# Optimization experiments

Hardware: AMD Instinct MI355X
Metric: run time of the kernel (lower is better)

## Reference

```python
import jax, jax.numpy as jnp
import numpy as np

B, N, D = 4, 1024, 1024      # batch, seq_len, d_model
H, DK, DV = 16, 64, 64       # n_head, d_k, d_v


def setup_inputs() -> dict:
    key = jax.random.key(0)
    ks = jax.random.split(key, 6)
    xavier = (2.0 / (D + DK)) ** 0.5  # xavier_normal_ std for (d_model, d_k) fan
    return {
        "q": jax.random.normal(ks[0], (B, N, D), jnp.float32),
        "k": jax.random.normal(ks[1], (B, N, D), jnp.float32),
        "v": jax.random.normal(ks[2], (B, N, D), jnp.float32),
        "weight_qs": xavier * jax.random.normal(ks[3], (H, D, DK), jnp.float32),
        "weight_ks": xavier * jax.random.normal(ks[4], (H, D, DK), jnp.float32),
        "weight_vs": xavier * jax.random.normal(ks[5], (H, D, DV), jnp.float32),
    }


def reference(q, k, v, weight_qs, weight_ks, weight_vs):
    # Per-head projections (torch: repeat batch over heads + bmm with (H,D,DK) weights)
    h, d_model, d_k = weight_qs.shape
    scale = 1.0 / (d_k ** 0.5)
    qh = jnp.einsum('bnd,hdk->hbnk', q, weight_qs)   # (H,B,N,DK)
    kh = jnp.einsum('bmd,hdk->hbmk', k, weight_ks)   # (H,B,M,DK)
    vh = jnp.einsum('bmd,hdv->hbmv', v, weight_vs)   # (H,B,M,DV)
    scores = jnp.einsum('hbnk,hbmk->hbnm', qh, kh) * scale  # (H,B,N,M)
    attn = jax.nn.softmax(scores, axis=-1)
    # dropout is identity in eval/deterministic mode
    out = jnp.einsum('hbnm,hbmv->hbnv', attn, vh)    # (H,B,N,DV)
    # torch: split head-stacked batch dim and cat along feature dim -> (B,N,H*DV)
    out = jnp.transpose(out, (1, 2, 0, 3)).reshape(out.shape[1], out.shape[2], -1)
    attn = attn.reshape(h * attn.shape[1], attn.shape[2], attn.shape[3])  # (H*B,N,M)
    return out, attn
```

## Files before the change

### kernel.cpp

```cpp
#include <hip/hip_runtime.h>

typedef short short8 __attribute__((ext_vector_type(8)));
typedef short short4_ __attribute__((ext_vector_type(4)));
typedef float f32x4 __attribute__((ext_vector_type(4)));

#define GLD16(gsrc, ldst) \
  __builtin_amdgcn_global_load_lds((__attribute__((address_space(1))) const void*)(gsrc), \
                                   (__attribute__((address_space(3))) void*)(ldst), 16, 0, 0)

#define BAR() do { asm volatile("s_waitcnt lgkmcnt(0)" ::: "memory"); \
  __builtin_amdgcn_sched_barrier(0); __builtin_amdgcn_s_barrier(); } while (0)

static __device__ __forceinline__ short f2bf(float f) {
  union { float f; unsigned u; } x; x.f = f;
  unsigned r = x.u + 0x7fffu + ((x.u >> 16) & 1u);
  return (short)(r >> 16);
}
static __device__ __forceinline__ float bf2f(unsigned short h) {
  union { unsigned u; float f; } x; x.u = ((unsigned)h) << 16;
  return x.f;
}

__global__ __launch_bounds__(256) void cast_qkv(
    const float* __restrict__ q, const float* __restrict__ k, const float* __restrict__ v,
    short* __restrict__ xq, short* __restrict__ xk, short* __restrict__ xv) {
  int z = blockIdx.z;
  const float* s = (z == 0) ? q : (z == 1) ? k : v;
  short* d = (z == 0) ? xq : (z == 1) ? xk : xv;
  int i = (blockIdx.x * 256 + threadIdx.x) * 4;
  float4 f = *(const float4*)(s + i);
  short4_ o;
  o[0] = f2bf(f.x); o[1] = f2bf(f.y); o[2] = f2bf(f.z); o[3] = f2bf(f.w);
  *(short4_*)(d + i) = o;
}

__global__ __launch_bounds__(256) void pack_w(
    const float* __restrict__ wq, const float* __restrict__ wk, const float* __restrict__ wv,
    short* __restrict__ oq, short* __restrict__ ok, short* __restrict__ ov) {
  int z = blockIdx.z;
  const float* W = (z == 0) ? wq : (z == 1) ? wk : wv;
  short* o = ((z == 0) ? oq : (z == 1) ? ok : ov) + (size_t)blockIdx.x * 1024;
  int c = blockIdx.x;
  int h = c >> 6, kk = c & 63;
  const float* src = W + (size_t)h * 65536 + kk;
  #pragma unroll
  for (int it = 0; it < 4; ++it) {
    int d = it * 256 + threadIdx.x;
    o[d] = f2bf(src[(size_t)d * 64]);
  }
}

__global__ __launch_bounds__(256) void proj_gemm(
    const short* __restrict__ xq, const short* __restrict__ xk, const short* __restrict__ xv,
    const short* __restrict__ wq, const short* __restrict__ wk, const short* __restrict__ wv,
    short* __restrict__ pq, short* __restrict__ pk, short* __restrict__ pv) {
  int z = blockIdx.z;
  const short* A  = (z == 0) ? xq : (z == 1) ? xk : xv;
  const short* Bt = (z == 0) ? wq : (z == 1) ? wk : wv;
  short* C        = (z == 0) ? pq : (z == 1) ? pk : pv;
  __shared__ __attribute__((aligned(16))) short As[128 * 32];
  __shared__ __attribute__((aligned(16))) short Bs[128 * 32];
  int t = threadIdx.x, l = t & 63, w = t >> 6;
  int wr = w >> 1, wc = w & 1;
  int lr = l & 15, lk = l >> 4;
  int bm0 = blockIdx.y * 128, bn0 = blockIdx.x * 128;
  const f32x4 Z = {0.f, 0.f, 0.f, 0.f};
  f32x4 acc[4][4];
  #pragma unroll
  for (int m = 0; m < 4; ++m)
    #pragma unroll
    for (int n = 0; n < 4; ++n) acc[m][n] = Z;

  int boff0 = w * 2 * 1024 + l * 16;
  int row0 = boff0 >> 6, ke0 = (boff0 & 63) >> 1;
  int boff1 = boff0 + 1024;
  int row1 = boff1 >> 6, ke1 = (boff1 & 63) >> 1;
  const short* ga0 = A + (size_t)(bm0 + row0) * 1024 + ke0;
  const short* ga1 = A + (size_t)(bm0 + row1) * 1024 + ke1;
  const short* gb0 = Bt + (size_t)(bn0 + row0) * 1024 + ke0;
  const short* gb1 = Bt + (size_t)(bn0 + row1) * 1024 + ke1;
  short* lA0 = As + (w * 2) * 512;     short* lA1 = As + (w * 2 + 1) * 512;
  short* lB0 = Bs + (w * 2) * 512;     short* lB1 = Bs + (w * 2 + 1) * 512;

  for (int kb = 0; kb < 1024; kb += 32) {
    GLD16(ga0 + kb, lA0);
    GLD16(ga1 + kb, lA1);
    GLD16(gb0 + kb, lB0);
    GLD16(gb1 + kb, lB1);
    __syncthreads();
    short8 a[4], bfr[4];
    #pragma unroll
    for (int m = 0; m < 4; ++m)
      a[m] = *(const short8*)(As + (wr * 64 + m * 16 + lr) * 32 + lk * 8);
    #pragma unroll
    for (int n = 0; n < 4; ++n)
      bfr[n] = *(const short8*)(Bs + (wc * 64 + n * 16 + lr) * 32 + lk * 8);
    __builtin_amdgcn_s_setprio(1);
    #pragma unroll
    for (int m = 0; m < 4; ++m)
      #pragma unroll
      for (int n = 0; n < 4; ++n)
        acc[m][n] = __builtin_amdgcn_mfma_f32_16x16x32_bf16(a[m], bfr[n], acc[m][n], 0, 0, 0);
    __builtin_amdgcn_s_setprio(0);
    __syncthreads();
  }
  #pragma unroll
  for (int m = 0; m < 4; ++m)
    #pragma unroll
    for (int n = 0; n < 4; ++n)
      #pragma unroll
      for (int i = 0; i < 4; ++i) {
        int r = bm0 + wr * 64 + m * 16 + lk * 4 + i;
        int cc = bn0 + wc * 64 + n * 16 + lr;
        C[(size_t)r * 1024 + cc] = f2bf(acc[m][n][i]);
      }
}

__global__ __launch_bounds__(256) void vtrans(
    const short* __restrict__ pv, short* __restrict__ vt) {
  __shared__ short T[64 * 72];
  int t = threadIdx.x;
  int hb = blockIdx.y, h = hb >> 2, b = hb & 3;
  int n0 = blockIdx.x * 64;
  const short* src = pv + (size_t)b * 1048576 + (size_t)n0 * 1024 + h * 64;
  #pragma unroll
  for (int it = 0; it < 2; ++it) {
    int id = it * 256 + t;
    int row = id >> 3, seg = id & 7;
    *(short8*)(T + row * 72 + seg * 8) = *(const short8*)(src + (size_t)row * 1024 + seg * 8);
  }
  __syncthreads();
  short* dst = vt + (size_t)hb * 65536 + n0;
  #pragma unroll
  for (int it = 0; it < 2; ++it) {
    int id = it * 256 + t;
    int dv = id >> 3, seg = id & 7;
    short8 vv;
    #pragma unroll
    for (int jj = 0; jj < 8; ++jj) vv[jj] = T[(seg * 8 + jj) * 72 + dv];
    *(short8*)(dst + (size_t)dv * 1024 + seg * 8) = vv;
  }
}

#define PW 72
__global__ __launch_bounds__(512) void attn_fused(
    const short* __restrict__ pq, const short* __restrict__ pk, const short* __restrict__ vt,
    float* __restrict__ dout) {
  __shared__ __attribute__((aligned(16))) short Ks[2][64 * PW];
  __shared__ __attribute__((aligned(16))) short Vs[2][64 * PW];
  __shared__ __attribute__((aligned(16))) short Ps[128 * PW];
  int t = threadIdx.x, l = t & 63, w = t >> 6;
  int lr = l & 15, lk = l >> 4;
  int bid = blockIdx.x;
  int swz = (bid & 7) * 64 + (bid >> 3);
  int hb = swz >> 3, qt = swz & 7;
  int h = hb >> 2, b = hb & 3;
  int q0 = qt * 128;
  const short* Qg = pq + (size_t)b * 1048576 + h * 64;
  const short* Kg = pk + (size_t)b * 1048576 + h * 64;
  const short* Vt = vt + (size_t)hb * 65536;
  float* attnp = dout + 4194304 + (size_t)hb * 1048576;
  const f32x4 Z = {0.f, 0.f, 0.f, 0.f};
  const float scale = 0.125f;
  int r0 = w * 16;
  int sj = t >> 3, sco = (t & 7) * 8;

  const short* qrow = Qg + (size_t)(q0 + r0 + lr) * 1024;
  short8 aq[2];
  aq[0] = *(const short8*)(qrow + lk * 8);
  aq[1] = *(const short8*)(qrow + 32 + lk * 8);

  short8 ka, va;
  ka = *(const short8*)(Kg + (size_t)sj * 1024 + sco);
  *(short8*)(Ks[0] + sj * PW + sco) = ka;
  BAR();

  float s[4] = {0.f, 0.f, 0.f, 0.f};

  for (int nc = 0; nc < 16; ++nc) {
    int cur = nc & 1;
    if (nc < 15)
      ka = *(const short8*)(Kg + (size_t)((nc + 1) * 64 + sj) * 1024 + sco);
    f32x4 acc[4] = {Z, Z, Z, Z};
    __builtin_amdgcn_s_setprio(1);
    #pragma unroll
    for (int kk = 0; kk < 2; ++kk)
      #pragma unroll
      for (int n = 0; n < 4; ++n) {
        short8 bk = *(const short8*)(Ks[cur] + (n * 16 + lr) * PW + kk * 32 + lk * 8);
        acc[n] = __builtin_amdgcn_mfma_f32_16x16x32_bf16(aq[kk], bk, acc[n], 0, 0, 0);
      }
    __builtin_amdgcn_s_setprio(0);
    #pragma unroll
    for (int i = 0; i < 4; ++i)
      s[i] += __expf(acc[0][i] * scale) + __expf(acc[1][i] * scale) +
              __expf(acc[2][i] * scale) + __expf(acc[3][i] * scale);
    if (nc < 15)
      *(short8*)(Ks[cur ^ 1] + sj * PW + sco) = ka;
    BAR();
  }
  #pragma unroll
  for (int i = 0; i < 4; ++i)
    #pragma unroll
    for (int msk = 1; msk < 16; msk <<= 1)
      s[i] += __shfl_xor(s[i], msk, 64);
  float inv[4];
  #pragma unroll
  for (int i = 0; i < 4; ++i) inv[i] = 1.0f / s[i];

  ka = *(const short8*)(Kg + (size_t)sj * 1024 + sco);
  va = *(const short8*)(Vt + (size_t)sj * 1024 + sco);
  *(short8*)(Ks[0] + sj * PW + sco) = ka;
  *(short8*)(Vs[0] + sj * PW + sco) = va;
  BAR();

  f32x4 acco[4] = {Z, Z, Z, Z};
  int prow = r0 + (l >> 2), pseg = (l & 3) * 16;
  float* gpb = attnp + (size_t)(q0 + prow) * 1024 + pseg;
  for (int nc = 0; nc < 16; ++nc) {
    int cur = nc & 1;
    if (nc < 15) {
      ka = *(const short8*)(Kg + (size_t)((nc + 1) * 64 + sj) * 1024 + sco);
      va = *(const short8*)(Vt + (size_t)sj * 1024 + (nc + 1) * 64 + sco);
    }
    f32x4 acc[4] = {Z, Z, Z, Z};
    __builtin_amdgcn_s_setprio(1);
    #pragma unroll
    for (int kk = 0; kk < 2; ++kk)
      #pragma unroll
      for (int n = 0; n < 4; ++n) {
        short8 bk = *(const short8*)(Ks[cur] + (n * 16 + lr) * PW + kk * 32 + lk * 8);
        acc[n] = __builtin_amdgcn_mfma_f32_16x16x32_bf16(aq[kk], bk, acc[n], 0, 0, 0);
      }
    __builtin_amdgcn_s_setprio(0);
    #pragma unroll
    for (int n = 0; n < 4; ++n)
      #pragma unroll
      for (int i = 0; i < 4; ++i) {
        float p = __expf(acc[n][i] * scale) * inv[i];
        Ps[(r0 + lk * 4 + i) * PW + n * 16 + lr] = f2bf(p);
      }
    #pragma unroll
    for (int kk = 0; kk < 2; ++kk) {
      short8 ap = *(const short8*)(Ps + (r0 + lr) * PW + kk * 32 + lk * 8);
      __builtin_amdgcn_s_setprio(1);
      #pragma unroll
      for (int f = 0; f < 4; ++f) {
        short8 bv = *(const short8*)(Vs[cur] + (f * 16 + lr) * PW + kk * 32 + lk * 8);
        acco[f] = __builtin_amdgcn_mfma_f32_16x16x32_bf16(ap, bv, acco[f], 0, 0, 0);
      }
      __builtin_amdgcn_s_setprio(0);
    }
    {
      short8 p0 = *(const short8*)(Ps + prow * PW + pseg);
      short8 p1 = *(const short8*)(Ps + prow * PW + pseg + 8);
      float* gp = gpb + nc * 64;
      float4 f0 = {bf2f((unsigned short)p0[0]), bf2f((unsigned short)p0[1]),
                   bf2f((unsigned short)p0[2]), bf2f((unsigned short)p0[3])};
      float4 f1 = {bf2f((unsigned short)p0[4]), bf2f((unsigned short)p0[5]),
                   bf2f((unsigned short)p0[6]), bf2f((unsigned short)p0[7])};
      float4 f2 = {bf2f((unsigned short)p1[0]), bf2f((unsigned short)p1[1]),
                   bf2f((unsigned short)p1[2]), bf2f((unsigned short)p1[3])};
      float4 f3 = {bf2f((unsigned short)p1[4]), bf2f((unsigned short)p1[5]),
                   bf2f((unsigned short)p1[6]), bf2f((unsigned short)p1[7])};
      *(float4*)gp = f0; *(float4*)(gp + 4) = f1;
      *(float4*)(gp + 8) = f2; *(float4*)(gp + 12) = f3;
    }
    if (nc < 15) {
      *(short8*)(Ks[cur ^ 1] + sj * PW + sco) = ka;
      *(short8*)(Vs[cur ^ 1] + sj * PW + sco) = va;
    }
    BAR();
  }
  #pragma unroll
  for (int f = 0; f < 4; ++f)
    #pragma unroll
    for (int i = 0; i < 4; ++i) {
      int row = q0 + r0 + lk * 4 + i;
      int dv = f * 16 + lr;
      dout[(size_t)b * 1048576 + (size_t)row * 1024 + h * 64 + dv] = acco[f][i];
    }
}

extern "C" void kernel_launch(void* const* d_in, const int* in_sizes, int n_in,
                              void* d_out, int out_size, void* d_ws, size_t ws_size,
                              hipStream_t stream) {
  const void* big[3] = {0, 0, 0};
  const void* small[3] = {0, 0, 0};
  int nb = 0, ns = 0;
  for (int i = 0; i < n_in && i < 6; ++i) {
    if (in_sizes[i] == 4194304) { if (nb < 3) big[nb++] = d_in[i]; }
    else                        { if (ns < 3) small[ns++] = d_in[i]; }
  }
  const float *q, *k, *v, *wq, *wk, *wv;
  if (nb == 3 && ns == 3) {
    q = (const float*)big[0]; k = (const float*)big[1]; v = (const float*)big[2];
    wq = (const float*)small[0]; wk = (const float*)small[1]; wv = (const float*)small[2];
  } else {
    q = (const float*)d_in[0]; k = (const float*)d_in[1]; v = (const float*)d_in[2];
    wq = (const float*)d_in[3]; wk = (const float*)d_in[4]; wv = (const float*)d_in[5];
  }
  short* W   = (short*)d_ws;
  short* xq  = W;
  short* xk  = W + 4194304;
  short* xv  = W + 8388608;
  short* wtq = W + 12582912;
  short* wtk = W + 13631488;
  short* wtv = W + 14680064;
  short* pq  = W + 15728640;
  short* pk  = W + 19922944;
  short* pv  = W + 24117248;
  short* vt  = W + 28311552;
  float* out = (float*)d_out;

  cast_qkv<<<dim3(4096, 1, 3), 256, 0, stream>>>(q, k, v, xq, xk, xv);
  pack_w<<<dim3(1024, 1, 3), 256, 0, stream>>>(wq, wk, wv, wtq, wtk, wtv);
  proj_gemm<<<dim3(8, 32, 3), 256, 0, stream>>>(xq, xk, xv, wtq, wtk, wtv, pq, pk, pv);
  vtrans<<<dim3(16, 64), 256, 0, stream>>>(pv, vt);
  attn_fused<<<dim3(512), 512, 0, stream>>>(pq, pk, vt, out);
}
```

Before: 190.8 us.

## Fuse V transpose into projection GEMM epilogue and deepen K/V prefetch

The separate vtrans kernel is removed. The projection GEMM now writes V directly in transposed per-head layout from its epilogue, which saves one kernel launch and a full round trip of the projected V through memory. In the attention kernel, K and V tile loads are now prefetched two tiles ahead through an extra register stage, to hide more global load latency. The transposed epilogue stores are scattered short writes, which may coalesce poorly, and the extra prefetch registers add register pressure.

```diff
diff --git a/kernel.cpp b/kernel.cpp
--- a/kernel.cpp
+++ b/kernel.cpp
@@ -53,11 +53,10 @@
 __global__ __launch_bounds__(256) void proj_gemm(
     const short* __restrict__ xq, const short* __restrict__ xk, const short* __restrict__ xv,
     const short* __restrict__ wq, const short* __restrict__ wk, const short* __restrict__ wv,
-    short* __restrict__ pq, short* __restrict__ pk, short* __restrict__ pv) {
+    short* __restrict__ pq, short* __restrict__ pk, short* __restrict__ vt) {
   int z = blockIdx.z;
   const short* A  = (z == 0) ? xq : (z == 1) ? xk : xv;
   const short* Bt = (z == 0) ? wq : (z == 1) ? wk : wv;
-  short* C        = (z == 0) ? pq : (z == 1) ? pk : pv;
   __shared__ __attribute__((aligned(16))) short As[128 * 32];
   __shared__ __attribute__((aligned(16))) short Bs[128 * 32];
   int t = threadIdx.x, l = t & 63, w = t >> 6;
@@ -112,34 +111,15 @@
       for (int i = 0; i < 4; ++i) {
         int r = bm0 + wr * 64 + m * 16 + lk * 4 + i;
         int cc = bn0 + wc * 64 + n * 16 + lr;
-        C[(size_t)r * 1024 + cc] = f2bf(acc[m][n][i]);
-      }
-}
-
-__global__ __launch_bounds__(256) void vtrans(
-    const short* __restrict__ pv, short* __restrict__ vt) {
-  __shared__ short T[64 * 72];
-  int t = threadIdx.x;
-  int hb = blockIdx.y, h = hb >> 2, b = hb & 3;
-  int n0 = blockIdx.x * 64;
-  const short* src = pv + (size_t)b * 1048576 + (size_t)n0 * 1024 + h * 64;
-  #pragma unroll
-  for (int it = 0; it < 2; ++it) {
-    int id = it * 256 + t;
-    int row = id >> 3, seg = id & 7;
-    *(short8*)(T + row * 72 + seg * 8) = *(const short8*)(src + (size_t)row * 1024 + seg * 8);
-  }
-  __syncthreads();
-  short* dst = vt + (size_t)hb * 65536 + n0;
-  #pragma unroll
-  for (int it = 0; it < 2; ++it) {
-    int id = it * 256 + t;
-    int dv = id >> 3, seg = id & 7;
-    short8 vv;
-    #pragma unroll
-    for (int jj = 0; jj < 8; ++jj) vv[jj] = T[(seg * 8 + jj) * 72 + dv];
-    *(short8*)(dst + (size_t)dv * 1024 + seg * 8) = vv;
-  }
+        short val = f2bf(acc[m][n][i]);
+        if (z == 2) {
+          int b = r >> 10, n1024 = r & 1023, h = cc >> 6, dv = cc & 63;
+          vt[(size_t)(h * 4 + b) * 65536 + (size_t)dv * 1024 + n1024] = val;
+        } else {
+          short* C = (z == 0) ? pq : pk;
+          C[(size_t)r * 1024 + cc] = val;
+        }
+      }
 }
 
 #define PW 72
@@ -170,17 +150,18 @@
   aq[0] = *(const short8*)(qrow + lk * 8);
   aq[1] = *(const short8*)(qrow + 32 + lk * 8);
 
-  short8 ka, va;
-  ka = *(const short8*)(Kg + (size_t)sj * 1024 + sco);
-  *(short8*)(Ks[0] + sj * PW + sco) = ka;
+  short8 ka_w, ka_n, va_w, va_n;
+  ka_w = *(const short8*)(Kg + (size_t)sj * 1024 + sco);
+  *(short8*)(Ks[0] + sj * PW + sco) = ka_w;
+  ka_w = *(const short8*)(Kg + (size_t)(64 + sj) * 1024 + sco);
   BAR();
 
   float s[4] = {0.f, 0.f, 0.f, 0.f};
 
   for (int nc = 0; nc < 16; ++nc) {
     int cur = nc & 1;
-    if (nc < 15)
-      ka = *(const short8*)(Kg + (size_t)((nc + 1) * 64 + sj) * 1024 + sco);
+    if (nc < 14)
+      ka_n = *(const short8*)(Kg + (size_t)((nc + 2) * 64 + sj) * 1024 + sco);
     f32x4 acc[4] = {Z, Z, Z, Z};
     __builtin_amdgcn_s_setprio(1);
     #pragma unroll
@@ -195,8 +176,10 @@
     for (int i = 0; i < 4; ++i)
       s[i] += __expf(acc[0][i] * scale) + __expf(acc[1][i] * scale) +
               __expf(acc[2][i] * scale) + __expf(acc[3][i] * scale);
-    if (nc < 15)
-      *(short8*)(Ks[cur ^ 1] + sj * PW + sco) = ka;
+    if (nc < 15) {
+      *(short8*)(Ks[cur ^ 1] + sj * PW + sco) = ka_w;
+      ka_w = ka_n;
+    }
     BAR();
   }
   #pragma unroll
@@ -208,10 +191,12 @@
   #pragma unroll
   for (int i = 0; i < 4; ++i) inv[i] = 1.0f / s[i];
 
-  ka = *(const short8*)(Kg + (size_t)sj * 1024 + sco);
-  va = *(const short8*)(Vt + (size_t)sj * 1024 + sco);
-  *(short8*)(Ks[0] + sj * PW + sco) = ka;
-  *(short8*)(Vs[0] + sj * PW + sco) = va;
+  ka_w = *(const short8*)(Kg + (size_t)sj * 1024 + sco);
+  va_w = *(const short8*)(Vt + (size_t)sj * 1024 + sco);
+  *(short8*)(Ks[0] + sj * PW + sco) = ka_w;
+  *(short8*)(Vs[0] + sj * PW + sco) = va_w;
+  ka_w = *(const short8*)(Kg + (size_t)(64 + sj) * 1024 + sco);
+  va_w = *(const short8*)(Vt + (size_t)sj * 1024 + 64 + sco);
   BAR();
 
   f32x4 acco[4] = {Z, Z, Z, Z};
@@ -219,9 +204,9 @@
   float* gpb = attnp + (size_t)(q0 + prow) * 1024 + pseg;
   for (int nc = 0; nc < 16; ++nc) {
     int cur = nc & 1;
-    if (nc < 15) {
-      ka = *(const short8*)(Kg + (size_t)((nc + 1) * 64 + sj) * 1024 + sco);
-      va = *(const short8*)(Vt + (size_t)sj * 1024 + (nc + 1) * 64 + sco);
+    if (nc < 14) {
+      ka_n = *(const short8*)(Kg + (size_t)((nc + 2) * 64 + sj) * 1024 + sco);
+      va_n = *(const short8*)(Vt + (size_t)sj * 1024 + (nc + 2) * 64 + sco);
     }
     f32x4 acc[4] = {Z, Z, Z, Z};
     __builtin_amdgcn_s_setprio(1);
@@ -267,8 +252,9 @@
       *(float4*)(gp + 8) = f2; *(float4*)(gp + 12) = f3;
     }
     if (nc < 15) {
-      *(short8*)(Ks[cur ^ 1] + sj * PW + sco) = ka;
-      *(short8*)(Vs[cur ^ 1] + sj * PW + sco) = va;
+      *(short8*)(Ks[cur ^ 1] + sj * PW + sco) = ka_w;
+      *(short8*)(Vs[cur ^ 1] + sj * PW + sco) = va_w;
+      ka_w = ka_n; va_w = va_n;
     }
     BAR();
   }
@@ -309,13 +295,11 @@
   short* wtv = W + 14680064;
   short* pq  = W + 15728640;
   short* pk  = W + 19922944;
-  short* pv  = W + 24117248;
   short* vt  = W + 28311552;
   float* out = (float*)d_out;
 
   cast_qkv<<<dim3(4096, 1, 3), 256, 0, stream>>>(q, k, v, xq, xk, xv);
   pack_w<<<dim3(1024, 1, 3), 256, 0, stream>>>(wq, wk, wv, wtq, wtk, wtv);
-  proj_gemm<<<dim3(8, 32, 3), 256, 0, stream>>>(xq, xk, xv, wtq, wtk, wtv, pq, pk, pv);
-  vtrans<<<dim3(16, 64), 256, 0, stream>>>(pv, vt);
+  proj_gemm<<<dim3(8, 32, 3), 256, 0, stream>>>(xq, xk, xv, wtq, wtk, wtv, pq, pk, vt);
   attn_fused<<<dim3(512), 512, 0, stream>>>(pq, pk, vt, out);
 }
```

Measured after the change: 208.6 us. 1.09x slower.

## Halve attention block to 256 threads with two 16-row tiles per wave

Applied to the files above, without the earlier changes.

Each wave now computes 32 query rows as two 16-row MFMA tiles that share every K and V fragment read from LDS, and the block shrinks from 8 to 4 waves for the same 128-row tile. Each thread stages two short8 chunks of K/V per step instead of one, and the attention-probability writeout covers 32 columns per lane. The aim is to halve the LDS reads of K/V per MFMA and raise instruction-level parallelism per wave. In exchange, register pressure per wave rises and fewer waves are resident to hide latency.

```diff
diff --git a/kernel.cpp b/kernel.cpp
--- a/kernel.cpp
+++ b/kernel.cpp
@@ -143,7 +143,7 @@
 }
 
 #define PW 72
-__global__ __launch_bounds__(512) void attn_fused(
+__global__ __launch_bounds__(256) void attn_fused(
     const short* __restrict__ pq, const short* __restrict__ pk, const short* __restrict__ vt,
     float* __restrict__ dout) {
   __shared__ __attribute__((aligned(16))) short Ks[2][64 * PW];
@@ -162,113 +162,139 @@
   float* attnp = dout + 4194304 + (size_t)hb * 1048576;
   const f32x4 Z = {0.f, 0.f, 0.f, 0.f};
   const float scale = 0.125f;
-  int r0 = w * 16;
-  int sj = t >> 3, sco = (t & 7) * 8;
-
-  const short* qrow = Qg + (size_t)(q0 + r0 + lr) * 1024;
-  short8 aq[2];
-  aq[0] = *(const short8*)(qrow + lk * 8);
-  aq[1] = *(const short8*)(qrow + 32 + lk * 8);
-
-  short8 ka, va;
-  ka = *(const short8*)(Kg + (size_t)sj * 1024 + sco);
-  *(short8*)(Ks[0] + sj * PW + sco) = ka;
+  int r0 = w * 32;
+  int sj = t >> 2, sc0 = (t & 3) * 16;
+
+  const short* qrowA = Qg + (size_t)(q0 + r0 + lr) * 1024;
+  const short* qrowB = Qg + (size_t)(q0 + r0 + 16 + lr) * 1024;
+  short8 aqA[2], aqB[2];
+  aqA[0] = *(const short8*)(qrowA + lk * 8);
+  aqA[1] = *(const short8*)(qrowA + 32 + lk * 8);
+  aqB[0] = *(const short8*)(qrowB + lk * 8);
+  aqB[1] = *(const short8*)(qrowB + 32 + lk * 8);
+
+  short8 ka0, ka1, va0, va1;
+  ka0 = *(const short8*)(Kg + (size_t)sj * 1024 + sc0);
+  ka1 = *(const short8*)(Kg + (size_t)sj * 1024 + sc0 + 8);
+  *(short8*)(Ks[0] + sj * PW + sc0) = ka0;
+  *(short8*)(Ks[0] + sj * PW + sc0 + 8) = ka1;
   BAR();
 
-  float s[4] = {0.f, 0.f, 0.f, 0.f};
+  float sA[4] = {0.f, 0.f, 0.f, 0.f}, sB[4] = {0.f, 0.f, 0.f, 0.f};
 
   for (int nc = 0; nc < 16; ++nc) {
     int cur = nc & 1;
-    if (nc < 15)
-      ka = *(const short8*)(Kg + (size_t)((nc + 1) * 64 + sj) * 1024 + sco);
-    f32x4 acc[4] = {Z, Z, Z, Z};
+    if (nc < 15) {
+      ka0 = *(const short8*)(Kg + (size_t)((nc + 1) * 64 + sj) * 1024 + sc0);
+      ka1 = *(const short8*)(Kg + (size_t)((nc + 1) * 64 + sj) * 1024 + sc0 + 8);
+    }
+    f32x4 accA[4] = {Z, Z, Z, Z}, accB[4] = {Z, Z, Z, Z};
     __builtin_amdgcn_s_setprio(1);
     #pragma unroll
     for (int kk = 0; kk < 2; ++kk)
       #pragma unroll
       for (int n = 0; n < 4; ++n) {
         short8 bk = *(const short8*)(Ks[cur] + (n * 16 + lr) * PW + kk * 32 + lk * 8);
-        acc[n] = __builtin_amdgcn_mfma_f32_16x16x32_bf16(aq[kk], bk, acc[n], 0, 0, 0);
+        accA[n] = __builtin_amdgcn_mfma_f32_16x16x32_bf16(aqA[kk], bk, accA[n], 0, 0, 0);
+        accB[n] = __builtin_amdgcn_mfma_f32_16x16x32_bf16(aqB[kk], bk, accB[n], 0, 0, 0);
       }
     __builtin_amdgcn_s_setprio(0);
     #pragma unroll
-    for (int i = 0; i < 4; ++i)
-      s[i] += __expf(acc[0][i] * scale) + __expf(acc[1][i] * scale) +
-              __expf(acc[2][i] * scale) + __expf(acc[3][i] * scale);
-    if (nc < 15)
-      *(short8*)(Ks[cur ^ 1] + sj * PW + sco) = ka;
+    for (int i = 0; i < 4; ++i) {
+      sA[i] += __expf(accA[0][i] * scale) + __expf(accA[1][i] * scale) +
+               __expf(accA[2][i] * scale) + __expf(accA[3][i] * scale);
+      sB[i] += __expf(accB[0][i] * scale) + __expf(accB[1][i] * scale) +
+               __expf(accB[2][i] * scale) + __expf(accB[3][i] * scale);
+    }
+    if (nc < 15) {
+      *(short8*)(Ks[cur ^ 1] + sj * PW + sc0) = ka0;
+      *(short8*)(Ks[cur ^ 1] + sj * PW + sc0 + 8) = ka1;
+    }
     BAR();
   }
   #pragma unroll
   for (int i = 0; i < 4; ++i)
     #pragma unroll
-    for (int msk = 1; msk < 16; msk <<= 1)
-      s[i] += __shfl_xor(s[i], msk, 64);
-  float inv[4];
-  #pragma unroll
-  for (int i = 0; i < 4; ++i) inv[i] = 1.0f / s[i];
-
-  ka = *(const short8*)(Kg + (size_t)sj * 1024 + sco);
-  va = *(const short8*)(Vt + (size_t)sj * 1024 + sco);
-  *(short8*)(Ks[0] + sj * PW + sco) = ka;
-  *(short8*)(Vs[0] + sj * PW + sco) = va;
+    for (int msk = 1; msk < 16; msk <<= 1) {
+      sA[i] += __shfl_xor(sA[i], msk, 64);
+      sB[i] += __shfl_xor(sB[i], msk, 64);
+    }
+  float invA[4], invB[4];
+  #pragma unroll
+  for (int i = 0; i < 4; ++i) { invA[i] = 1.0f / sA[i]; invB[i] = 1.0f / sB[i]; }
+
+  ka0 = *(const short8*)(Kg + (size_t)sj * 1024 + sc0);
+  ka1 = *(const short8*)(Kg + (size_t)sj * 1024 + sc0 + 8);
+  va0 = *(const short8*)(Vt + (size_t)sj * 1024 + sc0);
+  va1 = *(const short8*)(Vt + (size_t)sj * 1024 + sc0 + 8);
+  *(short8*)(Ks[0] + sj * PW + sc0) = ka0;
+  *(short8*)(Ks[0] + sj * PW + sc0 + 8) = ka1;
+  *(short8*)(Vs[0] + sj * PW + sc0) = va0;
+  *(short8*)(Vs[0] + sj * PW + sc0 + 8) = va1;
   BAR();
 
-  f32x4 acco[4] = {Z, Z, Z, Z};
-  int prow = r0 + (l >> 2), pseg = (l & 3) * 16;
+  f32x4 accoA[4] = {Z, Z, Z, Z}, accoB[4] = {Z, Z, Z, Z};
+  int prow = r0 + (l >> 1), pseg = (l & 1) * 32;
   float* gpb = attnp + (size_t)(q0 + prow) * 1024 + pseg;
   for (int nc = 0; nc < 16; ++nc) {
     int cur = nc & 1;
     if (nc < 15) {
-      ka = *(const short8*)(Kg + (size_t)((nc + 1) * 64 + sj) * 1024 + sco);
-      va = *(const short8*)(Vt + (size_t)sj * 1024 + (nc + 1) * 64 + sco);
-    }
-    f32x4 acc[4] = {Z, Z, Z, Z};
+      ka0 = *(const short8*)(Kg + (size_t)((nc + 1) * 64 + sj) * 1024 + sc0);
+      ka1 = *(const short8*)(Kg + (size_t)((nc + 1) * 64 + sj) * 1024 + sc0 + 8);
+      va0 = *(const short8*)(Vt + (size_t)sj * 1024 + (nc + 1) * 64 + sc0);
+      va1 = *(const short8*)(Vt + (size_t)sj * 1024 + (nc + 1) * 64 + sc0 + 8);
+    }
+    f32x4 accA[4] = {Z, Z, Z, Z}, accB[4] = {Z, Z, Z, Z};
     __builtin_amdgcn_s_setprio(1);
     #pragma unroll
     for (int kk = 0; kk < 2; ++kk)
       #pragma unroll
       for (int n = 0; n < 4; ++n) {
         short8 bk = *(const short8*)(Ks[cur] + (n * 16 + lr) * PW + kk * 32 + lk * 8);
-        acc[n] = __builtin_amdgcn_mfma_f32_16x16x32_bf16(aq[kk], bk, acc[n], 0, 0, 0);
+        accA[n] = __builtin_amdgcn_mfma_f32_16x16x32_bf16(aqA[kk], bk, accA[n], 0, 0, 0);
+        accB[n] = __builtin_amdgcn_mfma_f32_16x16x32_bf16(aqB[kk], bk, accB[n], 0, 0, 0);
       }
     __builtin_amdgcn_s_setprio(0);
     #pragma unroll
     for (int n = 0; n < 4; ++n)
       #pragma unroll
       for (int i = 0; i < 4; ++i) {
-        float p = __expf(acc[n][i] * scale) * inv[i];
-        Ps[(r0 + lk * 4 + i) * PW + n * 16 + lr] = f2bf(p);
+        float pA = __expf(accA[n][i] * scale) * invA[i];
+        float pB = __expf(accB[n][i] * scale) * invB[i];
+        Ps[(r0 + lk * 4 + i) * PW + n * 16 + lr] = f2bf(pA);
+        Ps[(r0 + 16 + lk * 4 + i) * PW + n * 16 + lr] = f2bf(pB);
       }
     #pragma unroll
     for (int kk = 0; kk < 2; ++kk) {
-      short8 ap = *(const short8*)(Ps + (r0 + lr) * PW + kk * 32 + lk * 8);
+      short8 apA = *(const short8*)(Ps + (r0 + lr) * PW + kk * 32 + lk * 8);
+      short8 apB = *(const short8*)(Ps + (r0 + 16 + lr) * PW + kk * 32 + lk * 8);
       __builtin_amdgcn_s_setprio(1);
       #pragma unroll
       for (int f = 0; f < 4; ++f) {
         short8 bv = *(const short8*)(Vs[cur] + (f * 16 + lr) * PW + kk * 32 + lk * 8);
-        acco[f] = __builtin_amdgcn_mfma_f32_16x16x32_bf16(ap, bv, acco[f], 0, 0, 0);
+        accoA[f] = __builtin_amdgcn_mfma_f32_16x16x32_bf16(apA, bv, accoA[f], 0, 0, 0);
+        accoB[f] = __builtin_amdgcn_mfma_f32_16x16x32_bf16(apB, bv, accoB[f], 0, 0, 0);
       }
       __builtin_amdgcn_s_setprio(0);
     }
     {
-      short8 p0 = *(const short8*)(Ps + prow * PW + pseg);
-      short8 p1 = *(const short8*)(Ps + prow * PW + pseg + 8);
       float* gp = gpb + nc * 64;
-      float4 f0 = {bf2f((unsigned short)p0[0]), bf2f((unsigned short)p0[1]),
-                   bf2f((unsigned short)p0[2]), bf2f((unsigned short)p0[3])};
-      float4 f1 = {bf2f((unsigned short)p0[4]), bf2f((unsigned short)p0[5]),
-                   bf2f((unsigned short)p0[6]), bf2f((unsigned short)p0[7])};
-      float4 f2 = {bf2f((unsigned short)p1[0]), bf2f((unsigned short)p1[1]),
-                   bf2f((unsigned short)p1[2]), bf2f((unsigned short)p1[3])};
-      float4 f3 = {bf2f((unsigned short)p1[4]), bf2f((unsigned short)p1[5]),
-                   bf2f((unsigned short)p1[6]), bf2f((unsigned short)p1[7])};
-      *(float4*)gp = f0; *(float4*)(gp + 4) = f1;
-      *(float4*)(gp + 8) = f2; *(float4*)(gp + 12) = f3;
+      #pragma unroll
+      for (int j = 0; j < 4; ++j) {
+        short8 p = *(const short8*)(Ps + prow * PW + pseg + j * 8);
+        float4 fo0 = {bf2f((unsigned short)p[0]), bf2f((unsigned short)p[1]),
+                      bf2f((unsigned short)p[2]), bf2f((unsigned short)p[3])};
+        float4 fo1 = {bf2f((unsigned short)p[4]), bf2f((unsigned short)p[5]),
+                      bf2f((unsigned short)p[6]), bf2f((unsigned short)p[7])};
+        *(float4*)(gp + j * 8) = fo0;
+        *(float4*)(gp + j * 8 + 4) = fo1;
+      }
     }
     if (nc < 15) {
-      *(short8*)(Ks[cur ^ 1] + sj * PW + sco) = ka;
-      *(short8*)(Vs[cur ^ 1] + sj * PW + sco) = va;
+      *(short8*)(Ks[cur ^ 1] + sj * PW + sc0) = ka0;
+      *(short8*)(Ks[cur ^ 1] + sj * PW + sc0 + 8) = ka1;
+      *(short8*)(Vs[cur ^ 1] + sj * PW + sc0) = va0;
+      *(short8*)(Vs[cur ^ 1] + sj * PW + sc0 + 8) = va1;
     }
     BAR();
   }
@@ -276,9 +302,10 @@
   for (int f = 0; f < 4; ++f)
     #pragma unroll
     for (int i = 0; i < 4; ++i) {
-      int row = q0 + r0 + lk * 4 + i;
+      int rowA = q0 + r0 + lk * 4 + i;
       int dv = f * 16 + lr;
-      dout[(size_t)b * 1048576 + (size_t)row * 1024 + h * 64 + dv] = acco[f][i];
+      dout[(size_t)b * 1048576 + (size_t)rowA * 1024 + h * 64 + dv] = accoA[f][i];
+      dout[(size_t)b * 1048576 + (size_t)(rowA + 16) * 1024 + h * 64 + dv] = accoB[f][i];
     }
 }
 
@@ -317,5 +344,5 @@
   pack_w<<<dim3(1024, 1, 3), 256, 0, stream>>>(wq, wk, wv, wtq, wtk, wtv);
   proj_gemm<<<dim3(8, 32, 3), 256, 0, stream>>>(xq, xk, xv, wtq, wtk, wtv, pq, pk, pv);
   vtrans<<<dim3(16, 64), 256, 0, stream>>>(pv, vt);
-  attn_fused<<<dim3(512), 512, 0, stream>>>(pq, pk, vt, out);
-}
+  attn_fused<<<dim3(512), 256, 0, stream>>>(pq, pk, vt, out);
+}
```

New measurement: 195.3 us. 1.02x slower.
